# Kernel tuning notes

Hardware: AMD Instinct MI355X
Metric: run time of the kernel (lower is better)

Reference implementation:

```python
import jax, jax.numpy as jnp
import numpy as np

NUM_NODES = 8192
MUL = 64
ENV_P = 6
EPSILON = 1.0 / np.sqrt(17.0)  # 1/sqrt(1 + avg_num_neighbors), avg_num_neighbors=16


def _envelope(u, p=ENV_P):
    # polynomial smoothing envelope (cutoff at u = 1)
    a = -(p + 1) * (p + 2) / 2.0
    b = p * (p + 2)
    c = -p * (p + 1) / 2.0
    f = 1.0 + a * u ** p + b * u ** (p + 1) + c * u ** (p + 2)
    return jnp.where(u < 1.0, f, 0.0)


def setup_inputs() -> dict:
    key = jax.random.key(0)
    ks = jax.random.split(key, 9)
    E, F = 131072, 512
    vectors = jax.random.normal(ks[0], (E, 3), jnp.float32) * 0.35  # mostly inside cutoff
    x = jax.random.normal(ks[1], (E, F), jnp.float32)
    V = jax.random.normal(ks[2], (E, MUL, 4), jnp.float32)  # per mul-channel: [0e | 1o(3)]
    senders = jax.random.randint(ks[3], (E,), 0, NUM_NODES, jnp.int32)
    W_w = jax.random.normal(ks[4], (F, MUL), jnp.float32)
    W1 = jax.random.normal(ks[5], (F + 2 * MUL, 512), jnp.float32)
    W2 = jax.random.normal(ks[6], (512, 512), jnp.float32)
    W3 = jax.random.normal(ks[7], (512, 512), jnp.float32)
    W_lin = jax.random.normal(ks[8], (3 * MUL, MUL), jnp.float32)
    return {"vectors": vectors, "x": x, "V": V, "senders": senders,
            "W_w": W_w, "W1": W1, "W2": W2, "W3": W3, "W_lin": W_lin}


def reference(vectors, x, V, senders, W_w, W1, W2, W3, W_lin):
    E = vectors.shape[0]
    # edge-wise linear producing tensor-product weights  [E, MUL]
    w = (x @ W_w) / np.sqrt(x.shape[-1])
    # spherical harmonics (component norm), l = 0..1 of normalized vectors -> [E, 4]
    r = jnp.linalg.norm(vectors, axis=-1, keepdims=True)          # [E, 1]
    nhat = vectors / r
    Y = jnp.concatenate([jnp.ones((E, 1), vectors.dtype), np.sqrt(3.0) * nhat], axis=1)
    # weighted SH, scatter-sum over senders, gather back (map_back=True), scale by epsilon
    wY_e = w[:, :, None] * Y[:, None, :]                          # [E, MUL, 4]
    agg = jax.ops.segment_sum(wY_e, senders, num_segments=NUM_NODES)
    wY = agg[senders] * EPSILON                                   # [E, MUL, 4]
    # CG tensor product wY (0e+1o) x V (0e+1o), keep 0e and 1o outputs
    a0, a1 = wY[..., 0], wY[..., 1:]
    b0, b1 = V[..., 0], V[..., 1:]
    scal = jnp.concatenate(
        [a0 * b0, jnp.einsum('emi,emi->em', a1, b1) / np.sqrt(3.0)], axis=-1)  # [E, 2*MUL]
    vecs = jnp.concatenate(
        [a0[..., None] * b1, a1 * b0[..., None], jnp.cross(a1, b1) / np.sqrt(2.0)],
        axis=1)                                                   # [E, 3*MUL, 3]
    # concat scalar channel into invariants, 3-layer MLP (silu, linear last)
    xc = jnp.concatenate([x, scal], axis=1)                       # [E, 640]
    h = jax.nn.silu(xc @ W1 / np.sqrt(xc.shape[-1]))
    h = jax.nn.silu(h @ W2 / np.sqrt(h.shape[-1]))
    h = h @ W3 / np.sqrt(h.shape[-1])
    x_out = _envelope(r) * h                                      # [E, 512]
    # equivariant linear over the 1o multiplicity axis
    V_out = jnp.einsum('ekc,km->emc', vecs, W_lin) / np.sqrt(vecs.shape[1])  # [E, MUL, 3]
    return x_out, V_out
```

## Files before the change

kernel.cpp:

```cpp
#include <hip/hip_runtime.h>
#include <cstdint>
#include <cstddef>

#define E_TOT 131072
#define NNODES 8192

typedef __attribute__((ext_vector_type(8))) short bf16x8;
typedef __attribute__((ext_vector_type(4))) float f32x4;
typedef unsigned short u16;
typedef unsigned int u32;

__device__ __forceinline__ u16 f2bf(float f) {
    u32 u = __builtin_bit_cast(u32, f);
    u32 r = (u + 0x7FFFu + ((u >> 16) & 1u)) >> 16;
    return (u16)r;
}

__device__ __forceinline__ void gload16(const u16* g, u16* l) {
    __builtin_amdgcn_global_load_lds((const __attribute__((address_space(1))) void*)g,
                                     (__attribute__((address_space(3))) void*)l, 16, 0, 0);
}

__device__ __forceinline__ bf16x8 lds_frag(const u16* base, int row, int bytecol) {
    return *(const bf16x8*)((const char*)base + row * 128 + (bytecol ^ ((row & 7) << 4)));
}

__global__ void wconv_kernel(const float* __restrict__ src, u16* __restrict__ dst,
                             int K, int N) {
    int idx = blockIdx.x * 256 + threadIdx.x;
    if (idx >= N * K) return;
    int n = idx / K, k = idx - n * K;
    dst[idx] = f2bf(src[(size_t)k * N + n]);
}

__global__ void xconv_kernel(const float4* __restrict__ x, ushort4* __restrict__ xb) {
    size_t i = (size_t)blockIdx.x * 256 + threadIdx.x;
    float4 v = x[i];
    ushort4 o;
    o.x = f2bf(v.x); o.y = f2bf(v.y); o.z = f2bf(v.z); o.w = f2bf(v.w);
    xb[i] = o;
}

__global__ void envy_kernel(const float* __restrict__ vectors, float* __restrict__ env,
                            float4* __restrict__ Y) {
    int e = blockIdx.x * 256 + threadIdx.x;
    float vx = vectors[3 * e + 0], vy = vectors[3 * e + 1], vz = vectors[3 * e + 2];
    float r2 = vx * vx + vy * vy + vz * vz;
    float r = sqrtf(r2);
    float u6 = r2 * r2 * r2;
    float f = 1.0f + u6 * (-28.0f + 48.0f * r - 21.0f * r2);
    env[e] = (r < 1.0f) ? f : 0.0f;
    float inv = 1.7320508075688772f / r;
    Y[e] = make_float4(1.0f, vx * inv, vy * inv, vz * inv);
}

__global__ void hist_kernel(const int* __restrict__ senders, int* __restrict__ cnt) {
    int e = blockIdx.x * 256 + threadIdx.x;
    atomicAdd(&cnt[senders[e]], 1);
}

__launch_bounds__(1024)
__global__ void scan_kernel(const int* __restrict__ cnt, int* __restrict__ off,
                            int* __restrict__ curs) {
    __shared__ int part[1024];
    const int t = threadIdx.x;
    int local[8];
    int s = 0;
#pragma unroll
    for (int j = 0; j < 8; ++j) { local[j] = cnt[t * 8 + j]; s += local[j]; }
    part[t] = s;
    __syncthreads();
    for (int d = 1; d < 1024; d <<= 1) {
        int v = (t >= d) ? part[t - d] : 0;
        __syncthreads();
        part[t] += v;
        __syncthreads();
    }
    int run = part[t] - s;
#pragma unroll
    for (int j = 0; j < 8; ++j) {
        off[t * 8 + j] = run;
        curs[t * 8 + j] = run;
        run += local[j];
    }
    if (t == 1023) off[8192] = run;
}

__global__ void permbuild_kernel(const int* __restrict__ senders, int* __restrict__ curs,
                                 int* __restrict__ perm) {
    int e = blockIdx.x * 256 + threadIdx.x;
    int s = senders[e];
    int p = atomicAdd(&curs[s], 1);
    perm[p] = e;
}

__launch_bounds__(256)
__global__ void gather_kernel(const float* __restrict__ w, const float4* __restrict__ Y,
                              const int* __restrict__ off, const int* __restrict__ perm,
                              float4* __restrict__ agg) {
    const int t = threadIdx.x;
    const int n = blockIdx.x * 4 + (t >> 6);
    const int m = t & 63;
    const int beg = off[n], end = off[n + 1];
    float4 acc = make_float4(0.f, 0.f, 0.f, 0.f);
    for (int i = beg; i < end; ++i) {
        int e = perm[i];
        float wv = w[(size_t)e * 64 + m];
        float4 y = Y[e];
        acc.x += wv * y.x; acc.y += wv * y.y; acc.z += wv * y.z; acc.w += wv * y.w;
    }
    agg[(size_t)n * 64 + m] = acc;
}

__launch_bounds__(256)
__global__ void wgemm_kernel(const u16* __restrict__ XB, const u16* __restrict__ Wt,
                             float* __restrict__ w) {
    __shared__ u16 As[128 * 72];
    __shared__ u16 Bs[64 * 72];
    const int e0 = blockIdx.x * 128;
    const int t = threadIdx.x, lane = t & 63, wid = t >> 6;
    const int lr = lane & 15, lh = lane >> 4;
    const int r8 = t >> 3, c8 = t & 7;
    f32x4 acc[2][4] = {};
    for (int kt = 0; kt < 8; ++kt) {
        const int kk = kt << 6;
#pragma unroll
        for (int i = 0; i < 4; ++i) {
            int row = i * 32 + r8;
            const u16* g = XB + (size_t)(e0 + row) * 512 + kk + c8 * 8;
            *(uint4*)((char*)As + row * 144 + c8 * 16) = *(const uint4*)g;
        }
#pragma unroll
        for (int i = 0; i < 2; ++i) {
            int row = i * 32 + r8;
            const u16* g = Wt + (size_t)row * 512 + kk + c8 * 8;
            *(uint4*)((char*)Bs + row * 144 + c8 * 16) = *(const uint4*)g;
        }
        __syncthreads();
#pragma unroll
        for (int k2 = 0; k2 < 2; ++k2) {
            bf16x8 af[2], bfr[4];
#pragma unroll
            for (int m = 0; m < 2; ++m)
                af[m] = *(const bf16x8*)((const char*)As + (wid * 32 + m * 16 + lr) * 144 + k2 * 64 + lh * 16);
#pragma unroll
            for (int n = 0; n < 4; ++n)
                bfr[n] = *(const bf16x8*)((const char*)Bs + (n * 16 + lr) * 144 + k2 * 64 + lh * 16);
#pragma unroll
            for (int m = 0; m < 2; ++m)
#pragma unroll
                for (int n = 0; n < 4; ++n)
                    acc[m][n] = __builtin_amdgcn_mfma_f32_16x16x32_bf16(af[m], bfr[n], acc[m][n], 0, 0, 0);
        }
        __syncthreads();
    }
    const float s = 0.044194173824159216f;
#pragma unroll
    for (int m = 0; m < 2; ++m)
#pragma unroll
        for (int n = 0; n < 4; ++n)
#pragma unroll
            for (int j = 0; j < 4; ++j) {
                int e = e0 + wid * 32 + m * 16 + lh * 4 + j;
                w[(size_t)e * 64 + n * 16 + lr] = acc[m][n][j] * s;
            }
}

__launch_bounds__(256)
__global__ void edge_kernel(const int* __restrict__ senders, const float4* __restrict__ agg4,
                            const float4* __restrict__ V4, const u16* __restrict__ Wlt,
                            u16* __restrict__ scal, float* __restrict__ Vout) {
    __shared__ u16 a_lds[3][32][200];
    __shared__ u16 w_lds[64 * 200];
    const int t = threadIdx.x;
    const int e0 = blockIdx.x * 32;
#pragma unroll
    for (int i = 0; i < 6; ++i) {
        int c = i * 256 + t;
        int row = c / 24, off = (c % 24) * 8;
        *(uint4*)((char*)w_lds + row * 400 + off * 2) = ((const uint4*)Wlt)[c];
    }
    const float invs3 = 0.5773502691896258f;
    const float invs2 = 0.7071067811865476f;
    const float EPS = 0.24253562503633297f;
#pragma unroll
    for (int i = 0; i < 8; ++i) {
        int el = i * 4 + (t >> 6);
        int m = t & 63;
        int e = e0 + el;
        int s = senders[e];
        float4 a = agg4[(size_t)s * 64 + m];
        a.x *= EPS; a.y *= EPS; a.z *= EPS; a.w *= EPS;
        float4 b = V4[(size_t)e * 64 + m];
        float s0 = a.x * b.x;
        float s1 = (a.y * b.y + a.z * b.z + a.w * b.w) * invs3;
        scal[(size_t)e * 128 + m] = f2bf(s0);
        scal[(size_t)e * 128 + 64 + m] = f2bf(s1);
        float cx = (a.z * b.w - a.w * b.z) * invs2;
        float cy = (a.w * b.y - a.y * b.w) * invs2;
        float cz = (a.y * b.z - a.z * b.y) * invs2;
        a_lds[0][el][m] = f2bf(a.x * b.y);
        a_lds[0][el][64 + m] = f2bf(a.y * b.x);
        a_lds[0][el][128 + m] = f2bf(cx);
        a_lds[1][el][m] = f2bf(a.x * b.z);
        a_lds[1][el][64 + m] = f2bf(a.z * b.x);
        a_lds[1][el][128 + m] = f2bf(cy);
        a_lds[2][el][m] = f2bf(a.x * b.w);
        a_lds[2][el][64 + m] = f2bf(a.w * b.x);
        a_lds[2][el][128 + m] = f2bf(cz);
    }
    __syncthreads();
    const int lane = t & 63, wid = t >> 6;
    const int lr = lane & 15, lh = lane >> 4;
    f32x4 acc[3][2] = {};
    for (int kt = 0; kt < 6; ++kt) {
        bf16x8 bfr = *(const bf16x8*)((const char*)w_lds + (wid * 16 + lr) * 400 + kt * 64 + lh * 16);
#pragma unroll
        for (int c = 0; c < 3; ++c)
#pragma unroll
            for (int m = 0; m < 2; ++m) {
                bf16x8 afr = *(const bf16x8*)((const char*)a_lds + ((c * 32 + m * 16 + lr) * 400) + kt * 64 + lh * 16);
                acc[c][m] = __builtin_amdgcn_mfma_f32_16x16x32_bf16(afr, bfr, acc[c][m], 0, 0, 0);
            }
    }
    __syncthreads();
    float* ot = (float*)a_lds;
    const float sc = 0.07216878364870323f;
#pragma unroll
    for (int c = 0; c < 3; ++c)
#pragma unroll
        for (int m = 0; m < 2; ++m)
#pragma unroll
            for (int j = 0; j < 4; ++j) {
                int row = m * 16 + lh * 4 + j;
                int mul = wid * 16 + lr;
                ot[row * 192 + mul * 3 + c] = acc[c][m][j] * sc;
            }
    __syncthreads();
    float4* vo = (float4*)(Vout + (size_t)e0 * 192);
#pragma unroll
    for (int i = 0; i < 6; ++i)
        vo[i * 256 + t] = ((float4*)ot)[i * 256 + t];
}

template <int MODE>
__launch_bounds__(512, 2)
__global__ void mlp_gemm(const u16* __restrict__ A, const u16* __restrict__ A2,
                         const u16* __restrict__ Bt, const int K, const float scale,
                         const float* __restrict__ env,
                         u16* __restrict__ outb, float* __restrict__ outf) {
    __shared__ u16 lds[2][2][256 * 64];
    const int nwg = gridDim.x;
    const int bid = blockIdx.x;
    const int swz = (bid & 7) * (nwg >> 3) + (bid >> 3);
    const int mt = swz >> 1, nt = swz & 1;
    const int e0 = mt << 8, n0 = nt << 8;
    const int t = threadIdx.x, lane = t & 63, wid = t >> 6;
    const int wm = wid >> 2, wn = wid & 3;
    const int lr = lane & 15, lh = lane >> 4;
    const int sr8 = lane >> 3;
    const int scol = ((lane & 7) ^ sr8) << 3;
    f32x4 acc[8][4] = {};
    const int nkt = K >> 6;

    for (int kt = 0; kt < nkt; ++kt) {
        if (kt == 0) {
            const int col = scol;
#pragma unroll
            for (int i = 0; i < 4; ++i) {
                const int row = e0 + i * 64 + wid * 8 + sr8;
                gload16(A + (size_t)row * 512 + col, &lds[0][0][i * 4096 + wid * 512]);
            }
#pragma unroll
            for (int i = 0; i < 4; ++i) {
                const int row = n0 + i * 64 + wid * 8 + sr8;
                gload16(Bt + (size_t)row * K + col, &lds[0][1][i * 4096 + wid * 512]);
            }
            __syncthreads();
        }
        if (kt + 1 < nkt) {
            const int kk = (kt + 1) << 6;
            const int col = kk + scol;
            const int nb = (kt + 1) & 1;
#pragma unroll
            for (int i = 0; i < 4; ++i) {
                const int row = e0 + i * 64 + wid * 8 + sr8;
                const u16* g;
                if (A2 && kk >= 512) g = A2 + (size_t)row * 128 + (col - 512);
                else                 g = A + (size_t)row * 512 + col;
                gload16(g, &lds[nb][0][i * 4096 + wid * 512]);
            }
#pragma unroll
            for (int i = 0; i < 4; ++i) {
                const int row = n0 + i * 64 + wid * 8 + sr8;
                gload16(Bt + (size_t)row * K + col, &lds[nb][1][i * 4096 + wid * 512]);
            }
        }
        const u16* Ab = lds[kt & 1][0];
        const u16* Bb = lds[kt & 1][1];
#pragma unroll
        for (int k2 = 0; k2 < 2; ++k2) {
            bf16x8 af[8], bfr[4];
#pragma unroll
            for (int m = 0; m < 8; ++m)
                af[m] = lds_frag(Ab, wm * 128 + m * 16 + lr, k2 * 64 + lh * 16);
#pragma unroll
            for (int n = 0; n < 4; ++n)
                bfr[n] = lds_frag(Bb, wn * 64 + n * 16 + lr, k2 * 64 + lh * 16);
#pragma unroll
            for (int m = 0; m < 8; ++m)
#pragma unroll
                for (int n = 0; n < 4; ++n)
                    acc[m][n] = __builtin_amdgcn_mfma_f32_16x16x32_bf16(af[m], bfr[n], acc[m][n], 0, 0, 0);
        }
        __syncthreads();
    }
#pragma unroll
    for (int m = 0; m < 8; ++m) {
#pragma unroll
        for (int j = 0; j < 4; ++j) {
            const int row = e0 + wm * 128 + m * 16 + lh * 4 + j;
            float ev = (MODE == 1) ? env[row] : 0.0f;
#pragma unroll
            for (int n = 0; n < 4; ++n) {
                const int col = n0 + wn * 64 + n * 16 + lr;
                float v = acc[m][n][j] * scale;
                if (MODE == 0) {
                    float sv = v / (1.0f + __expf(-v));
                    outb[(size_t)row * 512 + col] = f2bf(sv);
                } else {
                    outf[(size_t)row * 512 + col] = v * ev;
                }
            }
        }
    }
}

extern "C" void kernel_launch(void* const* d_in, const int* in_sizes, int n_in,
                              void* d_out, int out_size, void* d_ws, size_t ws_size,
                              hipStream_t stream) {
    const float* vectors = (const float*)d_in[0];
    const float* x       = (const float*)d_in[1];
    const float* V       = (const float*)d_in[2];
    const int*   senders = (const int*)d_in[3];
    const float* W_w     = (const float*)d_in[4];
    const float* W1      = (const float*)d_in[5];
    const float* W2      = (const float*)d_in[6];
    const float* W3      = (const float*)d_in[7];
    const float* W_lin   = (const float*)d_in[8];
    float* out = (float*)d_out;
    char* ws = (char*)d_ws;

    u16*    XB   = (u16*)(ws + 0x0);
    u16*    H1   = (u16*)(ws + 0x8000000);
    u16*    SCAL = (u16*)(ws + 0x10000000);
    float*  AGG  = (float*)(ws + 0x12000000);
    float*  ENV  = (float*)(ws + 0x12800000);
    float4* Yb   = (float4*)(ws + 0x12880000);
    float*  Wbuf = (float*)(ws + 0x12A80000);
    u16*    WT   = (u16*)(ws + 0x14A80000);
    u16* Wwt = WT;
    u16* W1t = Wwt + 64 * 512;
    u16* W2t = W1t + 512 * 640;
    u16* W3t = W2t + 512 * 512;
    u16* Wlt = W3t + 512 * 512;
    u16* H2 = XB;
    int* COUNT = (int*)(ws + 0x15000000);
    int* OFF   = (int*)(ws + 0x15010000);
    int* CURS  = (int*)(ws + 0x15020000);
    int* PERM  = (int*)(ws + 0x15030000);

    hipMemsetAsync(COUNT, 0, NNODES * sizeof(int), stream);

    wconv_kernel<<<(64 * 512) / 256, 256, 0, stream>>>(W_w, Wwt, 512, 64);
    wconv_kernel<<<(512 * 640) / 256, 256, 0, stream>>>(W1, W1t, 640, 512);
    wconv_kernel<<<(512 * 512) / 256, 256, 0, stream>>>(W2, W2t, 512, 512);
    wconv_kernel<<<(512 * 512) / 256, 256, 0, stream>>>(W3, W3t, 512, 512);
    wconv_kernel<<<(64 * 192) / 256, 256, 0, stream>>>(W_lin, Wlt, 192, 64);

    xconv_kernel<<<(E_TOT * 512 / 4) / 256, 256, 0, stream>>>((const float4*)x, (ushort4*)XB);
    envy_kernel<<<E_TOT / 256, 256, 0, stream>>>(vectors, ENV, Yb);

    hist_kernel<<<E_TOT / 256, 256, 0, stream>>>(senders, COUNT);
    scan_kernel<<<1, 1024, 0, stream>>>(COUNT, OFF, CURS);
    permbuild_kernel<<<E_TOT / 256, 256, 0, stream>>>(senders, CURS, PERM);

    wgemm_kernel<<<E_TOT / 128, 256, 0, stream>>>(XB, Wwt, Wbuf);
    gather_kernel<<<NNODES / 4, 256, 0, stream>>>(Wbuf, Yb, OFF, PERM, (float4*)AGG);

    edge_kernel<<<E_TOT / 32, 256, 0, stream>>>(senders, (const float4*)AGG, (const float4*)V,
                                                Wlt, SCAL, out + (size_t)E_TOT * 512);

    const float s640 = 0.03952847075210474f;
    const float s512 = 0.044194173824159216f;
    const int gemm_grid = (E_TOT / 256) * 2;
    mlp_gemm<0><<<gemm_grid, 512, 0, stream>>>(XB, SCAL, W1t, 640, s640, nullptr, H1, nullptr);
    mlp_gemm<0><<<gemm_grid, 512, 0, stream>>>(H1, nullptr, W2t, 512, s512, nullptr, H2, nullptr);
    mlp_gemm<1><<<gemm_grid, 512, 0, stream>>>(H2, nullptr, W3t, 512, s512, ENV, nullptr, out);
}
```

Before: 600.9 us.

## Deepen MLP GEMM prefetch to two tiles with vmcnt-based waits and setprio

Restructures the double-buffered K loop in the MLP GEMM so that two k-tiles are issued before the loop begins. Each iteration now waits with s_waitcnt vmcnt(8) instead of a full __syncthreads, so the next tile's global-to-LDS loads stay in flight while the current tile is computed. The following loads are issued only after all waves have finished reading the buffer they overwrite. MFMA sections are raised to priority 1 via s_setprio. This relies on hand-written waitcnt counts matching the eight loads per tile, and it uses raw barriers.

```diff
diff --git a/kernel.cpp b/kernel.cpp
--- a/kernel.cpp
+++ b/kernel.cpp
@@ -263,41 +263,32 @@
     f32x4 acc[8][4] = {};
     const int nkt = K >> 6;
 
+    auto issue = [&](int kt, int b) {
+        const int kk = kt << 6;
+        const int col = kk + scol;
+#pragma unroll
+        for (int i = 0; i < 4; ++i) {
+            const int row = e0 + i * 64 + wid * 8 + sr8;
+            const u16* g;
+            if (A2 && kk >= 512) g = A2 + (size_t)row * 128 + (col - 512);
+            else                 g = A + (size_t)row * 512 + col;
+            gload16(g, (u16*)&lds[b][0][i * 4096 + wid * 512]);
+        }
+#pragma unroll
+        for (int i = 0; i < 4; ++i) {
+            const int row = n0 + i * 64 + wid * 8 + sr8;
+            gload16(Bt + (size_t)row * K + col, (u16*)&lds[b][1][i * 4096 + wid * 512]);
+        }
+    };
+
+    issue(0, 0);
+    issue(1, 1);
     for (int kt = 0; kt < nkt; ++kt) {
-        if (kt == 0) {
-            const int col = scol;
-#pragma unroll
-            for (int i = 0; i < 4; ++i) {
-                const int row = e0 + i * 64 + wid * 8 + sr8;
-                gload16(A + (size_t)row * 512 + col, &lds[0][0][i * 4096 + wid * 512]);
-            }
-#pragma unroll
-            for (int i = 0; i < 4; ++i) {
-                const int row = n0 + i * 64 + wid * 8 + sr8;
-                gload16(Bt + (size_t)row * K + col, &lds[0][1][i * 4096 + wid * 512]);
-            }
-            __syncthreads();
-        }
-        if (kt + 1 < nkt) {
-            const int kk = (kt + 1) << 6;
-            const int col = kk + scol;
-            const int nb = (kt + 1) & 1;
-#pragma unroll
-            for (int i = 0; i < 4; ++i) {
-                const int row = e0 + i * 64 + wid * 8 + sr8;
-                const u16* g;
-                if (A2 && kk >= 512) g = A2 + (size_t)row * 128 + (col - 512);
-                else                 g = A + (size_t)row * 512 + col;
-                gload16(g, &lds[nb][0][i * 4096 + wid * 512]);
-            }
-#pragma unroll
-            for (int i = 0; i < 4; ++i) {
-                const int row = n0 + i * 64 + wid * 8 + sr8;
-                gload16(Bt + (size_t)row * K + col, &lds[nb][1][i * 4096 + wid * 512]);
-            }
-        }
+        if (kt + 1 < nkt) asm volatile("s_waitcnt vmcnt(8)\ns_barrier" ::: "memory");
+        else              asm volatile("s_waitcnt vmcnt(0)\ns_barrier" ::: "memory");
         const u16* Ab = lds[kt & 1][0];
         const u16* Bb = lds[kt & 1][1];
+        __builtin_amdgcn_s_setprio(1);
 #pragma unroll
         for (int k2 = 0; k2 < 2; ++k2) {
             bf16x8 af[8], bfr[4];
@@ -313,7 +304,11 @@
                 for (int n = 0; n < 4; ++n)
                     acc[m][n] = __builtin_amdgcn_mfma_f32_16x16x32_bf16(af[m], bfr[n], acc[m][n], 0, 0, 0);
         }
-        __syncthreads();
+        __builtin_amdgcn_s_setprio(0);
+        if (kt + 2 < nkt) {
+            asm volatile("s_waitcnt lgkmcnt(0)\ns_barrier" ::: "memory");
+            issue(kt + 2, kt & 1);
+        }
     }
 #pragma unroll
     for (int m = 0; m < 8; ++m) {
```

Result: no change. 602.0 us (+0.2%).
